# Kernel optimization log

Hardware: AMD Instinct MI355X
Metric: run time of the kernel (lower is better)

The kernel has to match this reference:

```python
import jax, jax.numpy as jnp
import numpy as np

N, D_IN, D_OUT, L, R = 32768, 2048, 2048, 8, 16
LORA_ALPHA, LORA_RANK = 32.0, 16.0
SCALE = LORA_ALPHA / LORA_RANK  # applied because alpha != rank


def setup_inputs() -> dict:
    key = jax.random.key(0)
    ks = jax.random.split(key, 6)
    x = jax.random.normal(ks[0], (N, D_IN), dtype=jnp.float32)
    W = jax.random.normal(ks[1], (D_OUT, D_IN), dtype=jnp.float32) * 0.02
    b = jax.random.normal(ks[2], (D_OUT,), dtype=jnp.float32) * 0.02
    A_all = jax.random.normal(ks[3], (L, R, D_IN), dtype=jnp.float32) * 0.02
    B_all = jax.random.normal(ks[4], (L, D_OUT, R), dtype=jnp.float32) * 0.02
    # per-sample adapter index; -1 would mean "no LoRA" (handled by mask below)
    lora_idx = jax.random.randint(ks[5], (N,), 0, L, dtype=jnp.int32)
    return {"x": x, "W": W, "b": b, "A_all": A_all, "B_all": B_all, "lora_idx": lora_idx}


def reference(x, W, b, A_all, B_all, lora_idx):
    # Base linear: base_layer(x) -> x @ W.T + b
    base_out = x @ W.T + b  # [N, D_OUT]
    # Multi-LoRA: per-token adapter selection. Instead of Python grouping
    # (gather-matmul-scatter per group), compute the tiny down-projection for
    # all adapters and mask-select, then one fused up-projection.
    u = jnp.einsum('nd,lrd->nlr', x, A_all)  # [N, L, R] (small: r=16)
    Lnum = A_all.shape[0]
    sel = (lora_idx[:, None] == jnp.arange(Lnum, dtype=lora_idx.dtype)[None, :]) \
          & (lora_idx >= 0)[:, None]  # [N, L] one-hot, zero row if idx < 0
    u = u * sel[:, :, None].astype(u.dtype) * jnp.asarray(SCALE, u.dtype)
    # delta[n] = scale * (x[n] @ A[idx_n].T) @ B[idx_n].T, zeros elsewhere
    delta = jnp.einsum('nlr,lor->no', u, B_all)  # [N, D_OUT]
    return base_out + delta
```

## Files before the change

kernel.cpp:

```cpp
#include <hip/hip_runtime.h>
#include <stdint.h>

#define N_TOK 32768
#define DIN   2048
#define DOUT  2048
#define LAD   8
#define RRK   16
#define KCAT  2176
#define SCALE 2.0f

typedef __attribute__((ext_vector_type(8))) short bf16x8;
typedef __attribute__((ext_vector_type(4))) float f32x4;

__device__ __forceinline__ unsigned short f2bf(float f) {
    union { float f; unsigned u; } c; c.f = f;
    return (unsigned short)((c.u + 0x7FFFu + ((c.u >> 16) & 1u)) >> 16);
}

__device__ __forceinline__ uint4 pack8(float4 a, float4 b) {
    union { unsigned short s[8]; uint4 v; } u;
    u.s[0] = f2bf(a.x); u.s[1] = f2bf(a.y); u.s[2] = f2bf(a.z); u.s[3] = f2bf(a.w);
    u.s[4] = f2bf(b.x); u.s[5] = f2bf(b.y); u.s[6] = f2bf(b.z); u.s[7] = f2bf(b.w);
    return u.v;
}

__device__ __forceinline__ bf16x8 cvt8(float4 a, float4 b) {
    union { uint4 v; bf16x8 h; } u;
    u.v = pack8(a, b);
    return u.h;
}

__device__ __forceinline__ void async16(const void* g, void* l) {
    __builtin_amdgcn_global_load_lds(
        (const __attribute__((address_space(1))) void*)g,
        (__attribute__((address_space(3))) void*)l, 16, 0, 0);
}

__global__ __launch_bounds__(256) void prep_w(const float* __restrict__ W,
                                              const float* __restrict__ A_all,
                                              const float* __restrict__ B_all,
                                              unsigned short* __restrict__ wcat,
                                              unsigned short* __restrict__ acat) {
    const int NW = DOUT * DIN / 8;
    const int NB = DOUT * LAD;
    const int NA = LAD * RRK * DIN / 8;
    int tid = blockIdx.x * 256 + threadIdx.x;
    if (tid < NW) {
        int e = tid * 8;
        int o = e / DIN, k = e % DIN;
        float4 f0 = *(const float4*)(W + e);
        float4 f1 = *(const float4*)(W + e + 4);
        *(uint4*)(wcat + (size_t)o * KCAT + k) = pack8(f0, f1);
    } else if (tid < NW + NB) {
        int t = tid - NW;
        int o = t >> 3, l = t & 7;
        const float* src = B_all + ((size_t)l * DOUT + o) * RRK;
        float4 f0 = *(const float4*)(src + 0);
        float4 f1 = *(const float4*)(src + 4);
        float4 f2 = *(const float4*)(src + 8);
        float4 f3 = *(const float4*)(src + 12);
        unsigned short* dst = wcat + (size_t)o * KCAT + DIN + l * RRK;
        *(uint4*)(dst + 0) = pack8(f0, f1);
        *(uint4*)(dst + 8) = pack8(f2, f3);
    } else if (tid < NW + NB + NA) {
        int e = (tid - NW - NB) * 8;
        float4 f0 = *(const float4*)(A_all + e);
        float4 f1 = *(const float4*)(A_all + e + 4);
        *(uint4*)(acat + e) = pack8(f0, f1);
    }
}

__global__ __launch_bounds__(512, 2) void xu_gemm(const float* __restrict__ x,
                                                  const unsigned short* __restrict__ acat,
                                                  const int* __restrict__ lidx,
                                                  unsigned short* __restrict__ xcat) {
    __shared__ short Bs[2][8192];
    const int tid = threadIdx.x;
    const int lane = tid & 63, wv = tid >> 6;
    const int quad = lane >> 4, lm = lane & 15;
    const int row0 = blockIdx.x * 128;

    const int rbase = wv * 8 + (lane >> 3);
    const int csrc = ((((lane & 7) * 16) ^ (((lane >> 3) & 7) << 4)) >> 1);

    auto stageB = [&](int kt, int buf) {
        short* dbase = &Bs[buf][0] + wv * 512;
#pragma unroll
        for (int j = 0; j < 2; ++j)
            async16(acat + (size_t)(j * 64 + rbase) * DIN + kt * 64 + csrc,
                    (void*)(dbase + j * 4096));
    };

    const int myrow = row0 + wv * 16 + lm;
    const float* gx = x + (size_t)myrow * DIN + quad * 8;
    unsigned short* gxc = xcat + (size_t)myrow * KCAT + quad * 8;

    f32x4 acc[8];
    f32x4 zero = {0.f, 0.f, 0.f, 0.f};
#pragma unroll
    for (int i = 0; i < 8; ++i) acc[i] = zero;

    stageB(0, 0);
    stageB(1, 1);
    asm volatile("s_waitcnt vmcnt(2)" ::: "memory");
    __builtin_amdgcn_s_barrier();

    for (int t = 0; t < 32; ++t) {
        const int buf = t & 1;
        bf16x8 bF[16];
#pragma unroll
        for (int nj = 0; nj < 8; ++nj)
#pragma unroll
            for (int ks = 0; ks < 2; ++ks) {
                const int rl = nj * 16 + lm;
                const int ob = (rl * 128 + ks * 64 + quad * 16) ^ ((lm & 7) << 4);
                bF[nj * 2 + ks] = *(const bf16x8*)((const char*)&Bs[buf][0] + ob);
            }
        float4 xa0 = *(const float4*)(gx + t * 64 + 0);
        float4 xa1 = *(const float4*)(gx + t * 64 + 4);
        float4 xb0 = *(const float4*)(gx + t * 64 + 32);
        float4 xb1 = *(const float4*)(gx + t * 64 + 36);
        asm volatile("s_waitcnt lgkmcnt(0)" ::: "memory");
        __builtin_amdgcn_s_barrier();
        stageB(t + 2 < 32 ? t + 2 : 31, buf);
        if (t < 31)
            asm volatile("s_waitcnt vmcnt(2)" ::: "memory");
        else
            asm volatile("s_waitcnt vmcnt(0)" ::: "memory");
        bf16x8 aF0 = cvt8(xa0, xa1);
        bf16x8 aF1 = cvt8(xb0, xb1);
        union { bf16x8 h; uint4 v; } s0, s1;
        s0.h = aF0; s1.h = aF1;
        *(uint4*)(gxc + t * 64 + 0)  = s0.v;
        *(uint4*)(gxc + t * 64 + 32) = s1.v;
#pragma unroll
        for (int nj = 0; nj < 8; ++nj) {
            acc[nj] = __builtin_amdgcn_mfma_f32_16x16x32_bf16(aF0, bF[nj * 2 + 0], acc[nj], 0, 0, 0);
            acc[nj] = __builtin_amdgcn_mfma_f32_16x16x32_bf16(aF1, bF[nj * 2 + 1], acc[nj], 0, 0, 0);
        }
        __builtin_amdgcn_s_barrier();
    }

#pragma unroll
    for (int e = 0; e < 4; ++e) {
        int t = row0 + wv * 16 + quad * 4 + e;
        int l = lidx[t];
#pragma unroll
        for (int nj = 0; nj < 8; ++nj) {
            float v = (nj == l) ? acc[nj][e] * SCALE : 0.0f;
            xcat[(size_t)t * KCAT + DIN + nj * 16 + lm] = f2bf(v);
        }
    }
}

#define BK2  64
#define NKT2 (KCAT / BK2)
#define NIT  (NKT2 / 2)

#define VMC4() asm volatile("s_waitcnt vmcnt(4)" ::: "memory")
#define VMC0() asm volatile("s_waitcnt vmcnt(0)" ::: "memory")
#define LGK8() asm volatile("s_waitcnt lgkmcnt(8)" ::: "memory")
#define LGK0() asm volatile("s_waitcnt lgkmcnt(0)" ::: "memory")
#define BARR() __builtin_amdgcn_s_barrier()
#define SBR()  __builtin_amdgcn_sched_barrier(0)
#define PRIO1() __builtin_amdgcn_s_setprio(1)
#define PRIO0() __builtin_amdgcn_s_setprio(0)

#define RD_A(D, QM)                                                            \
    _Pragma("unroll") for (int mi = 0; mi < 4; ++mi)                           \
    _Pragma("unroll") for (int ks = 0; ks < 2; ++ks) {                         \
        const int rl = ((QM) * 4 + mi) * 16 + lm;                              \
        const int ob = (rl * 128 + ks * 64 + quad * 16) ^ ((lm & 7) << 4);     \
        aF[mi * 2 + ks] = *(const bf16x8*)((const char*)&lds[D][wm][0] + ob);  \
    }

#define RD_B(D, QN, BF)                                                        \
    _Pragma("unroll") for (int ni = 0; ni < 2; ++ni)                           \
    _Pragma("unroll") for (int ks = 0; ks < 2; ++ks) {                         \
        const int rl = (wn & 1) * 64 + ((QN) * 2 + ni) * 16 + lm;              \
        const int ob = (rl * 128 + ks * 64 + quad * 16) ^ ((lm & 7) << 4);     \
        BF[ni * 2 + ks] =                                                      \
            *(const bf16x8*)((const char*)&lds[D][2 + (wn >> 1)][0] + ob);     \
    }

#define MFMA16(QM, QN, BF)                                                     \
    _Pragma("unroll") for (int mi = 0; mi < 4; ++mi)                           \
    _Pragma("unroll") for (int ni = 0; ni < 2; ++ni)                           \
    _Pragma("unroll") for (int ks = 0; ks < 2; ++ks)                           \
        acc[(QM) * 4 + mi][(QN) * 2 + ni] =                                    \
            __builtin_amdgcn_mfma_f32_16x16x32_bf16(                           \
                aF[mi * 2 + ks], BF[ni * 2 + ks],                              \
                acc[(QM) * 4 + mi][(QN) * 2 + ni], 0, 0, 0);

__global__ __launch_bounds__(512, 2) void gemm_main(const unsigned short* __restrict__ xcat,
                                                    const unsigned short* __restrict__ wcat,
                                                    const float* __restrict__ bias,
                                                    float* __restrict__ out) {
    __shared__ short lds[2][4][8192];
    const int tid = threadIdx.x;
    const int lane = tid & 63, wv = tid >> 6;
    const int wm = wv >> 2, wn = wv & 3;
    const int quad = lane >> 4, lm = lane & 15;

    const int orig = blockIdx.x;
    const int swz = (orig & 7) * ((int)gridDim.x >> 3) + (orig >> 3);
    const int col0 = (swz & 7) * 256;
    const int row0 = (swz >> 3) * 256;

    const int rbase = wv * 8 + (lane >> 3);
    const int csrc = ((((lane & 7) * 16) ^ (((lane >> 3) & 7) << 4)) >> 1);

    auto stage = [&](int buf, int part, int gk) {
        const int half = part & 1;
        const unsigned short* g = (part < 2)
            ? xcat + (size_t)(row0 + half * 128) * KCAT
            : wcat + (size_t)(col0 + half * 128) * KCAT;
        short* dbase = &lds[buf][part][0] + wv * 512;
#pragma unroll
        for (int j = 0; j < 2; ++j)
            async16(g + (size_t)(j * 64 + rbase) * KCAT + gk * 64 + csrc,
                    (void*)(dbase + j * 4096));
    };

    f32x4 acc[8][4];
    f32x4 zero = {0.f, 0.f, 0.f, 0.f};
#pragma unroll
    for (int i = 0; i < 8; ++i)
#pragma unroll
        for (int j = 0; j < 4; ++j) acc[i][j] = zero;

    bf16x8 aF[8];
    bf16x8 bF0[4], bF1[4];

    stage(0, 0, 0); stage(0, 1, 0); stage(0, 2, 0); stage(0, 3, 0);
    stage(1, 2, 1); stage(1, 3, 1);
    VMC4();
    BARR();
    RD_B(0, 0, bF0)

    for (int it = 0; it < NIT - 1; ++it) {
        RD_A(0, 0)
        stage(1, 0, 2 * it + 1); LGK8();
        BARR(); LGK0(); SBR(); PRIO1(); MFMA16(0, 0, bF0) PRIO0(); BARR();
        RD_B(0, 1, bF1)
        stage(1, 1, 2 * it + 1);
        BARR(); LGK0(); SBR(); PRIO1(); MFMA16(0, 1, bF1) PRIO0(); BARR();
        RD_A(0, 1)
        stage(0, 2, 2 * it + 2);
        BARR(); LGK0(); SBR(); PRIO1(); MFMA16(1, 1, bF1) PRIO0(); BARR();
        stage(0, 3, 2 * it + 2);
        BARR(); PRIO1(); MFMA16(1, 0, bF0) PRIO0(); VMC4();
        RD_B(1, 0, bF0)
        BARR();

        RD_A(1, 0)
        stage(0, 0, 2 * it + 2); LGK8();
        BARR(); LGK0(); SBR(); PRIO1(); MFMA16(0, 0, bF0) PRIO0(); BARR();
        RD_B(1, 1, bF1)
        stage(0, 1, 2 * it + 2);
        BARR(); LGK0(); SBR(); PRIO1(); MFMA16(0, 1, bF1) PRIO0(); BARR();
        RD_A(1, 1)
        stage(1, 2, 2 * it + 3);
        BARR(); LGK0(); SBR(); PRIO1(); MFMA16(1, 1, bF1) PRIO0(); BARR();
        stage(1, 3, 2 * it + 3);
        BARR(); PRIO1(); MFMA16(1, 0, bF0) PRIO0(); VMC4();
        RD_B(0, 0, bF0)
        BARR();
    }

    RD_A(0, 0)
    stage(1, 0, 2 * (NIT - 1) + 1); LGK8();
    BARR(); LGK0(); SBR(); PRIO1(); MFMA16(0, 0, bF0) PRIO0(); BARR();
    RD_B(0, 1, bF1)
    stage(1, 1, 2 * (NIT - 1) + 1);
    BARR(); LGK0(); SBR(); PRIO1(); MFMA16(0, 1, bF1) PRIO0(); BARR();
    RD_A(0, 1)
    BARR(); LGK0(); SBR(); PRIO1(); MFMA16(1, 1, bF1) PRIO0(); BARR();
    BARR(); PRIO1(); MFMA16(1, 0, bF0) PRIO0(); VMC0();
    RD_B(1, 0, bF0)
    BARR();
    RD_A(1, 0)
    BARR(); LGK0(); SBR(); PRIO1(); MFMA16(0, 0, bF0) PRIO0(); BARR();
    RD_B(1, 1, bF1)
    BARR(); LGK0(); SBR(); PRIO1(); MFMA16(0, 1, bF1) PRIO0(); BARR();
    RD_A(1, 1)
    BARR(); LGK0(); SBR(); PRIO1(); MFMA16(1, 1, bF1) PRIO0(); BARR();
    PRIO1(); MFMA16(1, 0, bF0) PRIO0();

#pragma unroll
    for (int ni = 0; ni < 4; ++ni) {
        int col = col0 + wn * 64 + ni * 16 + lm;
        float bv = bias[col];
#pragma unroll
        for (int mi = 0; mi < 8; ++mi) {
            int rbase2 = row0 + wm * 128 + mi * 16 + quad * 4;
#pragma unroll
            for (int e = 0; e < 4; ++e)
                out[(size_t)(rbase2 + e) * DOUT + col] = acc[mi][ni][e] + bv;
        }
    }
}

extern "C" void kernel_launch(void* const* d_in, const int* in_sizes, int n_in,
                              void* d_out, int out_size, void* d_ws, size_t ws_size,
                              hipStream_t stream) {
    const float* x     = (const float*)d_in[0];
    const float* W     = (const float*)d_in[1];
    const float* bias  = (const float*)d_in[2];
    const float* A_all = (const float*)d_in[3];
    const float* B_all = (const float*)d_in[4];
    const int*   lidx  = (const int*)d_in[5];
    float* out = (float*)d_out;

    char* ws = (char*)d_ws;
    unsigned short* xcat = (unsigned short*)ws;
    unsigned short* wcat = (unsigned short*)(ws + (size_t)N_TOK * KCAT * 2);
    unsigned short* acat = (unsigned short*)(ws + (size_t)N_TOK * KCAT * 2
                                                + (size_t)DOUT * KCAT * 2);

    prep_w<<<2240, 256, 0, stream>>>(W, A_all, B_all, wcat, acat);
    xu_gemm<<<N_TOK / 128, 512, 0, stream>>>(x, acat, lidx, xcat);
    gemm_main<<<dim3((N_TOK / 256) * (DOUT / 256)), 512, 0, stream>>>(xcat, wcat, bias, out);
}
```

Measured before the change: 772.7 us.

## Stage A-adapter tiles in 8-deep chunks and reorder MFMA chains by k-slice

The xu_gemm kernel drops its double-buffered, per-iteration barrier pipeline and instead loads eight K-tiles of the concatenated A matrix into a larger LDS buffer at once, with one wait and one barrier per chunk. The chunk's tiles are then consumed without further barriers, which cuts synchronisation overhead. The cost is no overlap between the A loads and compute, and LDS use grows from 32KB to 128KB, which may reduce occupancy. In the main GEMM the MFMA loop order is changed so that consecutive MFMAs write different accumulators, reducing dependent accumulator stalls.

```diff
diff --git a/kernel.cpp b/kernel.cpp
--- a/kernel.cpp
+++ b/kernel.cpp
@@ -74,7 +74,7 @@
                                                   const unsigned short* __restrict__ acat,
                                                   const int* __restrict__ lidx,
                                                   unsigned short* __restrict__ xcat) {
-    __shared__ short Bs[2][8192];
+    __shared__ short Bs[8][8192];
     const int tid = threadIdx.x;
     const int lane = tid & 63, wv = tid >> 6;
     const int quad = lane >> 4, lm = lane & 15;
@@ -83,14 +83,6 @@
     const int rbase = wv * 8 + (lane >> 3);
     const int csrc = ((((lane & 7) * 16) ^ (((lane >> 3) & 7) << 4)) >> 1);
 
-    auto stageB = [&](int kt, int buf) {
-        short* dbase = &Bs[buf][0] + wv * 512;
-#pragma unroll
-        for (int j = 0; j < 2; ++j)
-            async16(acat + (size_t)(j * 64 + rbase) * DIN + kt * 64 + csrc,
-                    (void*)(dbase + j * 4096));
-    };
-
     const int myrow = row0 + wv * 16 + lm;
     const float* gx = x + (size_t)myrow * DIN + quad * 8;
     unsigned short* gxc = xcat + (size_t)myrow * KCAT + quad * 8;
@@ -100,45 +92,48 @@
 #pragma unroll
     for (int i = 0; i < 8; ++i) acc[i] = zero;
 
-    stageB(0, 0);
-    stageB(1, 1);
-    asm volatile("s_waitcnt vmcnt(2)" ::: "memory");
-    __builtin_amdgcn_s_barrier();
-
-    for (int t = 0; t < 32; ++t) {
-        const int buf = t & 1;
-        bf16x8 bF[16];
-#pragma unroll
-        for (int nj = 0; nj < 8; ++nj)
-#pragma unroll
-            for (int ks = 0; ks < 2; ++ks) {
-                const int rl = nj * 16 + lm;
-                const int ob = (rl * 128 + ks * 64 + quad * 16) ^ ((lm & 7) << 4);
-                bF[nj * 2 + ks] = *(const bf16x8*)((const char*)&Bs[buf][0] + ob);
-            }
-        float4 xa0 = *(const float4*)(gx + t * 64 + 0);
-        float4 xa1 = *(const float4*)(gx + t * 64 + 4);
-        float4 xb0 = *(const float4*)(gx + t * 64 + 32);
-        float4 xb1 = *(const float4*)(gx + t * 64 + 36);
-        asm volatile("s_waitcnt lgkmcnt(0)" ::: "memory");
-        __builtin_amdgcn_s_barrier();
-        stageB(t + 2 < 32 ? t + 2 : 31, buf);
-        if (t < 31)
-            asm volatile("s_waitcnt vmcnt(2)" ::: "memory");
-        else
-            asm volatile("s_waitcnt vmcnt(0)" ::: "memory");
-        bf16x8 aF0 = cvt8(xa0, xa1);
-        bf16x8 aF1 = cvt8(xb0, xb1);
-        union { bf16x8 h; uint4 v; } s0, s1;
-        s0.h = aF0; s1.h = aF1;
-        *(uint4*)(gxc + t * 64 + 0)  = s0.v;
-        *(uint4*)(gxc + t * 64 + 32) = s1.v;
-#pragma unroll
-        for (int nj = 0; nj < 8; ++nj) {
-            acc[nj] = __builtin_amdgcn_mfma_f32_16x16x32_bf16(aF0, bF[nj * 2 + 0], acc[nj], 0, 0, 0);
-            acc[nj] = __builtin_amdgcn_mfma_f32_16x16x32_bf16(aF1, bF[nj * 2 + 1], acc[nj], 0, 0, 0);
+    for (int c = 0; c < 4; ++c) {
+        __syncthreads();
+#pragma unroll
+        for (int st = 0; st < 8; ++st) {
+            short* dbase = &Bs[st][0] + wv * 512;
+#pragma unroll
+            for (int j = 0; j < 2; ++j)
+                async16(acat + (size_t)(j * 64 + rbase) * DIN + (c * 8 + st) * 64 + csrc,
+                        (void*)(dbase + j * 4096));
         }
-        __builtin_amdgcn_s_barrier();
+        asm volatile("s_waitcnt vmcnt(0)" ::: "memory");
+        __syncthreads();
+
+#pragma unroll
+        for (int st = 0; st < 8; ++st) {
+            const int t = c * 8 + st;
+            float4 xa0 = *(const float4*)(gx + t * 64 + 0);
+            float4 xa1 = *(const float4*)(gx + t * 64 + 4);
+            float4 xb0 = *(const float4*)(gx + t * 64 + 32);
+            float4 xb1 = *(const float4*)(gx + t * 64 + 36);
+            bf16x8 aF0 = cvt8(xa0, xa1);
+            bf16x8 aF1 = cvt8(xb0, xb1);
+            union { bf16x8 h; uint4 v; } s0, s1;
+            s0.h = aF0; s1.h = aF1;
+            *(uint4*)(gxc + t * 64 + 0)  = s0.v;
+            *(uint4*)(gxc + t * 64 + 32) = s1.v;
+            bf16x8 bF[16];
+#pragma unroll
+            for (int nj = 0; nj < 8; ++nj)
+#pragma unroll
+                for (int ks = 0; ks < 2; ++ks) {
+                    const int rl = nj * 16 + lm;
+                    const int ob = (rl * 128 + ks * 64 + quad * 16) ^ ((lm & 7) << 4);
+                    bF[nj * 2 + ks] = *(const bf16x8*)((const char*)&Bs[st][0] + ob);
+                }
+#pragma unroll
+            for (int nj = 0; nj < 8; ++nj)
+                acc[nj] = __builtin_amdgcn_mfma_f32_16x16x32_bf16(aF0, bF[nj * 2 + 0], acc[nj], 0, 0, 0);
+#pragma unroll
+            for (int nj = 0; nj < 8; ++nj)
+                acc[nj] = __builtin_amdgcn_mfma_f32_16x16x32_bf16(aF1, bF[nj * 2 + 1], acc[nj], 0, 0, 0);
+        }
     }
 
 #pragma unroll
@@ -184,9 +179,9 @@
     }
 
 #define MFMA16(QM, QN, BF)                                                     \
+    _Pragma("unroll") for (int ks = 0; ks < 2; ++ks)                           \
     _Pragma("unroll") for (int mi = 0; mi < 4; ++mi)                           \
     _Pragma("unroll") for (int ni = 0; ni < 2; ++ni)                           \
-    _Pragma("unroll") for (int ks = 0; ks < 2; ++ks)                           \
         acc[(QM) * 4 + mi][(QN) * 2 + ni] =                                    \
             __builtin_amdgcn_mfma_f32_16x16x32_bf16(                           \
                 aF[mi * 2 + ks], BF[ni * 2 + ks],                              \
```

After: 771.3 us. About the same (-0.2%).
